# Performance work log

Hardware: AMD Instinct MI355X
Metric: run time of the kernel (lower is better)

Reference implementation:

```python
import jax, jax.numpy as jnp
import numpy as np

N = 8192
E = 131072
IN_DIM = 3000
HID = 512      # gcn1 out = HID // 2 = 256
OUT = 64
EPS = 1e-12


def gcn_conv(x, W, b, src, dst, n):
    """PyG GCNConv: add self-loops, symmetric norm, gather-matmul-scatter."""
    xw = x @ W                                   # [n, out]
    loop = jnp.arange(n, dtype=src.dtype)
    s = jnp.concatenate([src, loop])             # source j
    d = jnp.concatenate([dst, loop])             # target i
    deg = jax.ops.segment_sum(jnp.ones(s.shape[0], dtype=xw.dtype), d, num_segments=n)
    dinv = deg ** -0.5                           # deg >= 1 due to self-loops
    norm = dinv[s] * dinv[d]                     # [E+n]
    out = jax.ops.segment_sum(norm[:, None] * xw[s], d, num_segments=n)
    return out + b


def avg_readout(emb, mask):
    vsum = mask @ emb                            # [N, h]
    row_sum = jnp.sum(mask, axis=1, keepdims=True)
    g = vsum / row_sum
    nrm = jnp.maximum(jnp.linalg.norm(g, axis=1, keepdims=True), EPS)
    return g / nrm                               # F.normalize(p=2, dim=1)


def bilinear(h, c, Wd, bd):
    # nn.Bilinear(n_h, n_h, 1): out[n,o] = sum_ij h[n,i] Wd[o,i,j] c[n,j] + bd[o]
    return jnp.einsum('ni,oij,nj->no', h, Wd, c) + bd


def setup_inputs() -> dict:
    key = jax.random.key(0)
    k1, k2, k3, k4, k5, k6, k7 = jax.random.split(key, 7)
    gene_data = jax.random.normal(k1, (N, IN_DIM), dtype=jnp.float32)
    # sparse binary neighborhood mask (~16 neighbors/row) + self so row sums > 0
    mask = (jax.random.uniform(k2, (N, N)) < (16.0 / N)).astype(jnp.float32)
    mask = jnp.maximum(mask, jnp.eye(N, dtype=jnp.float32))
    spatial_edge_index = jax.random.randint(k3, (2, E), 0, N, dtype=jnp.int64)
    perm = jax.random.permutation(k4, N).astype(jnp.int64)
    h1 = HID // 2
    W1 = jax.random.normal(k5, (IN_DIM, h1), dtype=jnp.float32) / np.sqrt(IN_DIM)
    b1 = jnp.zeros((h1,), dtype=jnp.float32)
    W2 = jax.random.normal(k6, (h1, OUT), dtype=jnp.float32) / np.sqrt(h1)
    b2 = jnp.zeros((OUT,), dtype=jnp.float32)
    Wd = jax.random.normal(k7, (1, OUT, OUT), dtype=jnp.float32) / np.sqrt(OUT)
    bd = jnp.zeros((1,), dtype=jnp.float32)
    return {"gene_data": gene_data, "mask": mask, "W1": W1, "b1": b1,
            "W2": W2, "b2": b2, "Wd": Wd, "bd": bd,
            "spatial_edge_index": spatial_edge_index, "perm": perm}


def reference(gene_data, mask, W1, b1, W2, b2, Wd, bd, spatial_edge_index, perm):
    src, dst = spatial_edge_index[0], spatial_edge_index[1]
    n = gene_data.shape[0]
    x1 = gene_data
    x1_c = gene_data[perm]                       # permuted (corrupted) graph
    # dropout inactive (eval mode, p=0.0)
    x1 = jax.nn.relu(gcn_conv(x1, W1, b1, src, dst, n))
    x1_c = jax.nn.relu(gcn_conv(x1_c, W1, b1, src, dst, n))
    x1 = jax.nn.relu(gcn_conv(x1, W2, b2, src, dst, n))
    x1_c = jax.nn.relu(gcn_conv(x1_c, W2, b2, src, dst, n))
    g1 = jax.nn.sigmoid(avg_readout(x1, mask))
    g1_c = jax.nn.sigmoid(avg_readout(x1_c, mask))
    ret1 = jnp.concatenate([bilinear(x1, g1, Wd, bd), bilinear(x1_c, g1, Wd, bd)], axis=1)
    ret1_c = jnp.concatenate([bilinear(x1_c, g1_c, Wd, bd), bilinear(x1, g1_c, Wd, bd)], axis=1)
    return (x1, ret1, ret1_c)
```

## Files before the change

### kernel.cpp

```cpp
#include <hip/hip_runtime.h>
#include <hip/hip_bf16.h>

#define NN 8192
#define NMASK 8191
#define IND 3000
#define INDP 3008
#define H1 256
#define OUTD 64

typedef __bf16 bf16x8 __attribute__((ext_vector_type(8)));
typedef float floatx4 __attribute__((ext_vector_type(4)));

__device__ __forceinline__ unsigned short f2b(float f) {
    __hip_bfloat16 h = __float2bfloat16(f);
    unsigned short u;
    __builtin_memcpy(&u, &h, 2);
    return u;
}


__global__ void k_probe(float code, float* out) {
    if (threadIdx.x == 0 && blockIdx.x == 0) out[0] = code;
}


__global__ void k_pre(const unsigned* __restrict__ eraw, const unsigned* __restrict__ praw,
                      int* __restrict__ flags, int* __restrict__ deg,
                      const float* __restrict__ W1, const float* __restrict__ W2,
                      __hip_bfloat16* __restrict__ W1t, __hip_bfloat16* __restrict__ W2t) {
    int b = blockIdx.x;
    int t = threadIdx.x;
    if (b < 2) {
        const unsigned* r = (b == 0) ? eraw : praw;
        __shared__ int cnt;
        if (t == 0) cnt = 0;
        __syncthreads();
        int z = 0;
        for (int k = t; k < 2048; k += 256)
            if (r[2 * k + 1] == 0u) z++;
        atomicAdd(&cnt, z);
        __syncthreads();
        if (t == 0) flags[b] = (cnt > 1024) ? 1 : 0;
    } else if (b < 10) {
#pragma unroll
        for (int u = 0; u < 4; ++u) deg[(b - 2) * 1024 + u * 256 + t] = 0;
    } else if (b < 12) {
        int idx = (b - 10) * 256 + t;
#pragma unroll
        for (int u = 0; u < 4; ++u) {
            int k = idx * 4 + u;
            int c = k >> 3;
            int r = 3000 + (k & 7);
            W1t[(size_t)c * INDP + r] = __float2bfloat16(0.f);
        }
    } else {
        int idx = (b - 12) * 256 + t;
        if (idx < IND * H1) {
            int r = idx / H1, c = idx % H1;
            W1t[(size_t)c * INDP + r] = __float2bfloat16(W1[idx]);
        } else {
            int j = idx - IND * H1;
            if (j < H1 * OUTD) {
                int r = j / OUTD, c = j % OUTD;
                W2t[(size_t)c * H1 + r] = __float2bfloat16(W2[j]);
            }
        }
    }
}


__global__ void k_prep(const unsigned* __restrict__ eraw, const unsigned* __restrict__ praw,
                       const int* __restrict__ flags, int* __restrict__ eidx32,
                       int* __restrict__ perm32, int* __restrict__ deg, int E, int n) {
    int i = blockIdx.x * blockDim.x + threadIdx.x;
    if (i < 2 * E) {
        unsigned v = flags[0] ? eraw[2 * (size_t)i] : eraw[i];
        int x = (int)(v & (unsigned)NMASK);
        eidx32[i] = x;
        if (i >= E) atomicAdd(&deg[x], 1);
    } else {
        int j = i - 2 * E;
        if (j < n) {
            unsigned v = flags[1] ? praw[2 * (size_t)j] : praw[j];
            perm32[j] = (int)(v & (unsigned)NMASK);
        }
    }
}


__global__ __launch_bounds__(1024) void k_scan(const int* __restrict__ deg,
                                               int* __restrict__ row_ptr,
                                               int* __restrict__ cursor,
                                               float* __restrict__ dinv, int n) {
    __shared__ int sums[1024];
    int t = threadIdx.x;
    int per = n / 1024;
    int base = t * per;
    int s = 0;
    for (int u = 0; u < per; ++u) s += deg[base + u];
    sums[t] = s;
    __syncthreads();
    for (int off = 1; off < 1024; off <<= 1) {
        int v = (t >= off) ? sums[t - off] : 0;
        __syncthreads();
        sums[t] += v;
        __syncthreads();
    }
    int run = (t == 0) ? 0 : sums[t - 1];
    for (int u = 0; u < per; ++u) {
        int i = base + u;
        row_ptr[i] = run;
        cursor[i] = run;
        int d = deg[i];
        dinv[i] = rsqrtf((float)(1 + d));
        run += d;
    }
    if (t == 1023) row_ptr[n] = run;
}

__global__ void k_scatter(const int* __restrict__ src, const int* __restrict__ dst,
                          int* __restrict__ cursor, int* __restrict__ col, int E) {
    int e = blockIdx.x * blockDim.x + threadIdx.x;
    if (e < E) {
        int d = dst[e];
        int p = atomicAdd(&cursor[d], 1);
        if (p >= 0 && p < E) col[p] = src[e];
    }
}


__global__ __launch_bounds__(256) void k_gemm1(const float* __restrict__ A,
                                               const __hip_bfloat16* __restrict__ Bt,
                                               float* __restrict__ C) {
    __shared__ __align__(16) unsigned short As[64 * 72];
    __shared__ __align__(16) unsigned short Bs[64 * 72];
    int t = threadIdx.x;
    int n0 = blockIdx.x * 64;
    int m0 = blockIdx.y * 64;
    int lane = t & 63;
    int w = t >> 6;
    int srow = t >> 2;
    int schunk = (t & 3) * 16;
    const float* Arow = A + (size_t)(m0 + srow) * IND + schunk;
    const unsigned short* Brow = (const unsigned short*)Bt + (size_t)(n0 + srow) * INDP + schunk;

    floatx4 acc0 = {0.f, 0.f, 0.f, 0.f}, acc1 = acc0, acc2 = acc0, acc3 = acc0;
    int msub = w * 16;
    int arow = msub + (lane & 15);
    int koff = (lane >> 4) * 8;
    int nlo = lane & 15;

    float4 pa0, pa1, pa2, pa3;
    uint4 pb0, pb1;
    auto load_tile = [&](int k0) {
        float4 z4 = make_float4(0.f, 0.f, 0.f, 0.f);
        uint4 zu = make_uint4(0u, 0u, 0u, 0u);
        pa0 = z4; pa1 = z4; pa2 = z4; pa3 = z4; pb0 = zu; pb1 = zu;
        int kk = k0 + schunk;
        if (kk < IND) {
            const float* ap = Arow + k0;
            pa0 = *reinterpret_cast<const float4*>(ap);
            pa1 = *reinterpret_cast<const float4*>(ap + 4);
            pb0 = *reinterpret_cast<const uint4*>(Brow + k0);
        }
        if (kk + 8 < IND) {
            const float* ap = Arow + k0 + 8;
            pa2 = *reinterpret_cast<const float4*>(ap);
            pa3 = *reinterpret_cast<const float4*>(ap + 4);
            pb1 = *reinterpret_cast<const uint4*>(Brow + k0 + 8);
        }
    };
    load_tile(0);
    for (int k0 = 0; k0 < IND; k0 += 64) {
        uint4 av0, av1, bv0 = pb0, bv1 = pb1;
        {
            unsigned short t8[8] = {f2b(pa0.x), f2b(pa0.y), f2b(pa0.z), f2b(pa0.w),
                                    f2b(pa1.x), f2b(pa1.y), f2b(pa1.z), f2b(pa1.w)};
            __builtin_memcpy(&av0, t8, 16);
        }
        {
            unsigned short t8[8] = {f2b(pa2.x), f2b(pa2.y), f2b(pa2.z), f2b(pa2.w),
                                    f2b(pa3.x), f2b(pa3.y), f2b(pa3.z), f2b(pa3.w)};
            __builtin_memcpy(&av1, t8, 16);
        }
        __syncthreads();
        *reinterpret_cast<uint4*>(&As[srow * 72 + schunk]) = av0;
        *reinterpret_cast<uint4*>(&As[srow * 72 + schunk + 8]) = av1;
        *reinterpret_cast<uint4*>(&Bs[srow * 72 + schunk]) = bv0;
        *reinterpret_cast<uint4*>(&Bs[srow * 72 + schunk + 8]) = bv1;
        __syncthreads();
        if (k0 + 64 < IND) load_tile(k0 + 64);
#pragma unroll
        for (int ks = 0; ks < 64; ks += 32) {
            bf16x8 af = *reinterpret_cast<const bf16x8*>(&As[arow * 72 + ks + koff]);
            bf16x8 b0 = *reinterpret_cast<const bf16x8*>(&Bs[(0 + nlo) * 72 + ks + koff]);
            bf16x8 b1 = *reinterpret_cast<const bf16x8*>(&Bs[(16 + nlo) * 72 + ks + koff]);
            bf16x8 b2 = *reinterpret_cast<const bf16x8*>(&Bs[(32 + nlo) * 72 + ks + koff]);
            bf16x8 b3 = *reinterpret_cast<const bf16x8*>(&Bs[(48 + nlo) * 72 + ks + koff]);
            acc0 = __builtin_amdgcn_mfma_f32_16x16x32_bf16(af, b0, acc0, 0, 0, 0);
            acc1 = __builtin_amdgcn_mfma_f32_16x16x32_bf16(af, b1, acc1, 0, 0, 0);
            acc2 = __builtin_amdgcn_mfma_f32_16x16x32_bf16(af, b2, acc2, 0, 0, 0);
            acc3 = __builtin_amdgcn_mfma_f32_16x16x32_bf16(af, b3, acc3, 0, 0, 0);
        }
    }
    int crow = msub + (lane >> 4) * 4;
    int ccol = lane & 15;
    floatx4 accs[4] = {acc0, acc1, acc2, acc3};
#pragma unroll
    for (int j = 0; j < 4; ++j) {
#pragma unroll
        for (int r = 0; r < 4; ++r) {
            C[(size_t)(m0 + crow + r) * H1 + (n0 + j * 16 + ccol)] = accs[j][r];
        }
    }
}


__global__ __launch_bounds__(256) void k_gemm2(const __hip_bfloat16* __restrict__ A,
                                               const __hip_bfloat16* __restrict__ Bt,
                                               float* __restrict__ C,
                                               int M, int N, int K) {
    __shared__ __align__(16) unsigned short As[64 * 40];
    __shared__ __align__(16) unsigned short Bs[64 * 40];
    int t = threadIdx.x;
    int m0 = blockIdx.x * 64;
    int n0 = blockIdx.y * 64;
    int lane = t & 63;
    int w = t >> 6;
    int srow = t >> 2;
    int schunk = (t & 3) * 8;
    size_t aoff = (size_t)(m0 + srow) * K + schunk;
    const unsigned short* Brow = (const unsigned short*)Bt + (size_t)(n0 + srow) * K + schunk;

    floatx4 acc0 = {0.f, 0.f, 0.f, 0.f}, acc1 = acc0, acc2 = acc0, acc3 = acc0;
    int msub = w * 16;
    int arow = msub + (lane & 15);
    int koff = (lane >> 4) * 8;
    int nlo = lane & 15;

    uint4 pa = *reinterpret_cast<const uint4*>((const unsigned short*)A + aoff);
    uint4 pb = *reinterpret_cast<const uint4*>(Brow);
    for (int k0 = 0; k0 < K; k0 += 32) {
        uint4 av = pa, bv = pb;
        __syncthreads();
        *reinterpret_cast<uint4*>(&As[srow * 40 + schunk]) = av;
        *reinterpret_cast<uint4*>(&Bs[srow * 40 + schunk]) = bv;
        __syncthreads();
        if (k0 + 32 < K) {
            pa = *reinterpret_cast<const uint4*>((const unsigned short*)A + aoff + k0 + 32);
            pb = *reinterpret_cast<const uint4*>(Brow + k0 + 32);
        }
        bf16x8 af = *reinterpret_cast<const bf16x8*>(&As[arow * 40 + koff]);
        bf16x8 bf0 = *reinterpret_cast<const bf16x8*>(&Bs[(0 + nlo) * 40 + koff]);
        bf16x8 bf1 = *reinterpret_cast<const bf16x8*>(&Bs[(16 + nlo) * 40 + koff]);
        bf16x8 bf2 = *reinterpret_cast<const bf16x8*>(&Bs[(32 + nlo) * 40 + koff]);
        bf16x8 bf3 = *reinterpret_cast<const bf16x8*>(&Bs[(48 + nlo) * 40 + koff]);
        acc0 = __builtin_amdgcn_mfma_f32_16x16x32_bf16(af, bf0, acc0, 0, 0, 0);
        acc1 = __builtin_amdgcn_mfma_f32_16x16x32_bf16(af, bf1, acc1, 0, 0, 0);
        acc2 = __builtin_amdgcn_mfma_f32_16x16x32_bf16(af, bf2, acc2, 0, 0, 0);
        acc3 = __builtin_amdgcn_mfma_f32_16x16x32_bf16(af, bf3, acc3, 0, 0, 0);
    }
    int crow = msub + (lane >> 4) * 4;
    int ccol = lane & 15;
    floatx4 accs[4] = {acc0, acc1, acc2, acc3};
#pragma unroll
    for (int j = 0; j < 4; ++j) {
#pragma unroll
        for (int r = 0; r < 4; ++r) {
            C[(size_t)(m0 + crow + r) * N + (n0 + j * 16 + ccol)] = accs[j][r];
        }
    }
}


__global__ __launch_bounds__(256) void k_agg1(const float* __restrict__ xw1,
                                              const int* __restrict__ row_ptr,
                                              const int* __restrict__ col,
                                              const float* __restrict__ dinv,
                                              const int* __restrict__ perm,
                                              const float* __restrict__ b1,
                                              __hip_bfloat16* __restrict__ h_all, int n) {
    int lane = threadIdx.x & 63;
    int i = blockIdx.x * 4 + (threadIdx.x >> 6);
    float di = dinv[i];
    int pi = perm[i];
    float sw = di * di;
    int c4 = lane * 4;
    floatx4 acc = sw * *reinterpret_cast<const floatx4*>(xw1 + (size_t)i * H1 + c4);
    floatx4 accc = sw * *reinterpret_cast<const floatx4*>(xw1 + (size_t)pi * H1 + c4);
    int s = row_ptr[i], e = row_ptr[i + 1];
#pragma unroll 4
    for (int t = s; t < e; ++t) {
        int j = col[t];
        float wv = di * dinv[j];
        int pj = perm[j];
        acc += wv * *reinterpret_cast<const floatx4*>(xw1 + (size_t)j * H1 + c4);
        accc += wv * *reinterpret_cast<const floatx4*>(xw1 + (size_t)pj * H1 + c4);
    }
    floatx4 b4 = *reinterpret_cast<const floatx4*>(b1 + c4);
    ushort4 h0, h1;
    h0.x = f2b(fmaxf(acc[0] + b4[0], 0.f));
    h0.y = f2b(fmaxf(acc[1] + b4[1], 0.f));
    h0.z = f2b(fmaxf(acc[2] + b4[2], 0.f));
    h0.w = f2b(fmaxf(acc[3] + b4[3], 0.f));
    h1.x = f2b(fmaxf(accc[0] + b4[0], 0.f));
    h1.y = f2b(fmaxf(accc[1] + b4[1], 0.f));
    h1.z = f2b(fmaxf(accc[2] + b4[2], 0.f));
    h1.w = f2b(fmaxf(accc[3] + b4[3], 0.f));
    *reinterpret_cast<ushort4*>(h_all + (size_t)i * H1 + c4) = h0;
    *reinterpret_cast<ushort4*>(h_all + (size_t)(n + i) * H1 + c4) = h1;
}


__global__ __launch_bounds__(256) void k_agg2(const float* __restrict__ hw_all,
                                              const int* __restrict__ row_ptr,
                                              const int* __restrict__ col,
                                              const float* __restrict__ dinv,
                                              const float* __restrict__ b2,
                                              float* __restrict__ x1_all,
                                              float* __restrict__ out_x1, int n) {
    int lane = threadIdx.x & 63;
    int i = blockIdx.x * 4 + (threadIdx.x >> 6);
    float di = dinv[i];
    float sw = di * di;
    float acc = sw * hw_all[(size_t)i * OUTD + lane];
    float accc = sw * hw_all[(size_t)(n + i) * OUTD + lane];
    int s = row_ptr[i], e = row_ptr[i + 1];
#pragma unroll 4
    for (int t = s; t < e; ++t) {
        int j = col[t];
        float wv = di * dinv[j];
        acc += wv * hw_all[(size_t)j * OUTD + lane];
        accc += wv * hw_all[(size_t)(n + j) * OUTD + lane];
    }
    float b = b2[lane];
    float v = fmaxf(acc + b, 0.f);
    float vc = fmaxf(accc + b, 0.f);
    x1_all[(size_t)i * OUTD + lane] = v;
    x1_all[(size_t)(n + i) * OUTD + lane] = vc;
    out_x1[(size_t)i * OUTD + lane] = v;
}


__global__ __launch_bounds__(256) void k_readout(const float* __restrict__ mask,
                                                 const float* __restrict__ x1_all,
                                                 const float* __restrict__ Wd,
                                                 const float* __restrict__ bd,
                                                 float* __restrict__ ret1,
                                                 float* __restrict__ ret1c, int n) {
    int i = blockIdx.x;
    int lane = threadIdx.x & 63;
    int w = threadIdx.x >> 6;
    float acc = 0.f, accc = 0.f, rs = 0.f;
    const float* mrow = mask + (size_t)i * n;
    int quarter = n >> 2;
    int qbase = w * quarter;
    for (int it = 0; it < 4; ++it) {
        int jb = qbase + it * 512 + lane * 8;
        floatx4 q0 = __builtin_nontemporal_load(reinterpret_cast<const floatx4*>(mrow + jb));
        floatx4 q1 = __builtin_nontemporal_load(reinterpret_cast<const floatx4*>(mrow + jb + 4));
        float qa[8] = {q0[0], q0[1], q0[2], q0[3], q1[0], q1[1], q1[2], q1[3]};
        bool nz = false;
#pragma unroll
        for (int u = 0; u < 8; ++u) nz |= (qa[u] != 0.f);
        unsigned long long bal = __ballot(nz);
        while (bal) {
            int l = __builtin_ctzll(bal);
            bal &= bal - 1;
            int j0 = qbase + it * 512 + l * 8;
#pragma unroll
            for (int u = 0; u < 8; ++u) {
                float m = __shfl(qa[u], l);
                if (m != 0.f) {
                    int j = j0 + u;
                    acc += m * x1_all[(size_t)j * OUTD + lane];
                    accc += m * x1_all[(size_t)(n + j) * OUTD + lane];
                    rs += m;
                }
            }
        }
    }
    __shared__ float sa[4][64], sc[4][64], sr[4];
    sa[w][lane] = acc;
    sc[w][lane] = accc;
    if (lane == 0) sr[w] = rs;
    __syncthreads();
    if (w == 0) {
        float tot = sa[0][lane] + sa[1][lane] + sa[2][lane] + sa[3][lane];
        float totc = sc[0][lane] + sc[1][lane] + sc[2][lane] + sc[3][lane];
        float rst = fmaxf(sr[0] + sr[1] + sr[2] + sr[3], 1e-20f);
        float g = tot / rst;
        float gc = totc / rst;
        float s1 = g * g, s2 = gc * gc;
#pragma unroll
        for (int off = 32; off; off >>= 1) {
            s1 += __shfl_xor(s1, off);
            s2 += __shfl_xor(s2, off);
        }
        float gn = g / fmaxf(sqrtf(s1), 1e-12f);
        float gnc = gc / fmaxf(sqrtf(s2), 1e-12f);
        float gsig = 1.f / (1.f + __expf(-gn));
        float gcsig = 1.f / (1.f + __expf(-gnc));
        float tg = 0.f, tgc = 0.f;
        const float* wrow = Wd + lane * 64;
#pragma unroll 8
        for (int j = 0; j < 64; ++j) {
            float gj = __shfl(gsig, j);
            float gcj = __shfl(gcsig, j);
            float wv = wrow[j];
            tg += wv * gj;
            tgc += wv * gcj;
        }
        float x = x1_all[(size_t)i * OUTD + lane];
        float xc = x1_all[(size_t)(n + i) * OUTD + lane];
        float r0 = x * tg, r1 = xc * tg, r2 = xc * tgc, r3 = x * tgc;
#pragma unroll
        for (int off = 32; off; off >>= 1) {
            r0 += __shfl_down(r0, off);
            r1 += __shfl_down(r1, off);
            r2 += __shfl_down(r2, off);
            r3 += __shfl_down(r3, off);
        }
        if (lane == 0) {
            float b = bd[0];
            ret1[(size_t)i * 2 + 0] = r0 + b;
            ret1[(size_t)i * 2 + 1] = r1 + b;
            ret1c[(size_t)i * 2 + 0] = r2 + b;
            ret1c[(size_t)i * 2 + 1] = r3 + b;
        }
    }
}


extern "C" void kernel_launch(void* const* d_in, const int* in_sizes, int n_in,
                              void* d_out, int out_size, void* d_ws, size_t ws_size,
                              hipStream_t stream) {
    const float* gene = (const float*)d_in[0];
    const float* mask = (const float*)d_in[1];
    const float* W1 = (const float*)d_in[2];
    const float* b1 = (const float*)d_in[3];
    const float* W2 = (const float*)d_in[4];
    const float* b2 = (const float*)d_in[5];
    const float* Wd = (const float*)d_in[6];
    const float* bd = (const float*)d_in[7];
    const unsigned* eidx_raw = (const unsigned*)d_in[8];
    const unsigned* perm_raw = (const unsigned*)d_in[9];
    const int n = NN;
    const int E = in_sizes[8] / 2;

    char* base = (char*)d_ws;
    char* p = base;
    auto alloc = [&](size_t bytes) -> char* {
        char* r = p;
        p += (bytes + 255) & ~(size_t)255;
        return r;
    };
    int* flags = (int*)alloc(256);
    int* eidx32 = (int*)alloc((size_t)2 * E * 4);
    int* perm32 = (int*)alloc((size_t)n * 4);
    int* deg = (int*)alloc((size_t)n * 4);
    int* row_ptr = (int*)alloc((size_t)(n + 1) * 4);
    int* cursor = (int*)alloc((size_t)n * 4);
    float* dinv = (float*)alloc((size_t)n * 4);
    int* col = (int*)alloc((size_t)E * 4);
    __hip_bfloat16* W2t = (__hip_bfloat16*)alloc((size_t)H1 * OUTD * 2);
    __hip_bfloat16* W1t = (__hip_bfloat16*)alloc((size_t)INDP * H1 * 2);
    float* xw1 = (float*)alloc((size_t)n * H1 * 4);
    __hip_bfloat16* h_all = (__hip_bfloat16*)alloc((size_t)2 * n * H1 * 2);
    size_t need = (size_t)(p - base);
    float* hw_all = xw1;
    float* x1_all = xw1 + (size_t)2 * n * OUTD;

    float* out_x1 = (float*)d_out;
    float* out_ret1 = out_x1 + (size_t)n * OUTD;
    float* out_ret1c = out_ret1 + (size_t)n * 2;

    if (ws_size < need) {
        k_probe<<<1, 64, 0, stream>>>(1000.f + (float)(ws_size >> 20), out_x1);
        return;
    }

    k_pre<<<3076, 256, 0, stream>>>(eidx_raw, perm_raw, flags, deg, W1, W2, W1t, W2t);

    k_prep<<<(2 * E + n + 255) / 256, 256, 0, stream>>>(eidx_raw, perm_raw, flags,
                                                        eidx32, perm32, deg, E, n);
    const int* srcv = eidx32;
    const int* dstv = eidx32 + E;

    k_scan<<<1, 1024, 0, stream>>>(deg, row_ptr, cursor, dinv, n);
    k_scatter<<<(E + 255) / 256, 256, 0, stream>>>(srcv, dstv, cursor, col, E);

    k_gemm1<<<dim3(H1 / 64, n / 64), 256, 0, stream>>>(gene, W1t, xw1);

    k_agg1<<<n / 4, 256, 0, stream>>>(xw1, row_ptr, col, dinv, perm32, b1, h_all, n);

    k_gemm2<<<dim3(2 * n / 64, OUTD / 64), 256, 0, stream>>>(h_all, W2t, hw_all, 2 * n, OUTD, H1);

    k_agg2<<<n / 4, 256, 0, stream>>>(hw_all, row_ptr, col, dinv, b2, x1_all, out_x1, n);

    k_readout<<<n, 256, 0, stream>>>(mask, x1_all, Wd, bd, out_ret1, out_ret1c, n);
}
```

Baseline: 609.2 us.

## Pipeline mask rows through an LDS ring and compact nonzeros per wave

```diff
diff --git a/kernel.cpp b/kernel.cpp
--- a/kernel.cpp
+++ b/kernel.cpp
@@ -10,6 +10,9 @@
 
 typedef __bf16 bf16x8 __attribute__((ext_vector_type(8)));
 typedef float floatx4 __attribute__((ext_vector_type(4)));
+
+typedef const __attribute__((address_space(1))) void GV;
+typedef __attribute__((address_space(3))) void LV;
 
 __device__ __forceinline__ unsigned short f2b(float f) {
     __hip_bfloat16 h = __float2bfloat16(f);
@@ -348,86 +351,116 @@
                                                  const float* __restrict__ bd,
                                                  float* __restrict__ ret1,
                                                  float* __restrict__ ret1c, int n) {
-    int i = blockIdx.x;
+    __shared__ __align__(16) float ring[4][4][512];
+    __shared__ uint2 ents[4][256];
     int lane = threadIdx.x & 63;
     int w = threadIdx.x >> 6;
-    float acc = 0.f, accc = 0.f, rs = 0.f;
-    const float* mrow = mask + (size_t)i * n;
-    int quarter = n >> 2;
-    int qbase = w * quarter;
-    for (int it = 0; it < 4; ++it) {
-        int jb = qbase + it * 512 + lane * 8;
-        floatx4 q0 = __builtin_nontemporal_load(reinterpret_cast<const floatx4*>(mrow + jb));
-        floatx4 q1 = __builtin_nontemporal_load(reinterpret_cast<const floatx4*>(mrow + jb + 4));
-        float qa[8] = {q0[0], q0[1], q0[2], q0[3], q1[0], q1[1], q1[2], q1[3]};
-        bool nz = false;
-#pragma unroll
-        for (int u = 0; u < 8; ++u) nz |= (qa[u] != 0.f);
-        unsigned long long bal = __ballot(nz);
-        while (bal) {
-            int l = __builtin_ctzll(bal);
-            bal &= bal - 1;
-            int j0 = qbase + it * 512 + l * 8;
-#pragma unroll
-            for (int u = 0; u < 8; ++u) {
-                float m = __shfl(qa[u], l);
-                if (m != 0.f) {
-                    int j = j0 + u;
-                    acc += m * x1_all[(size_t)j * OUTD + lane];
-                    accc += m * x1_all[(size_t)(n + j) * OUTD + lane];
-                    rs += m;
-                }
+    int row = blockIdx.x * 4 + w;
+    const float* mrow = mask + (size_t)row * n;
+
+    auto issue = [&](int c) {
+        int slot = c & 3;
+        const float* g0 = mrow + c * 512 + lane * 4;
+        __builtin_amdgcn_global_load_lds((GV*)g0, (LV*)&ring[w][slot][0], 16, 0, 0);
+        __builtin_amdgcn_global_load_lds((GV*)(g0 + 256), (LV*)&ring[w][slot][256], 16, 0, 0);
+    };
+    issue(0);
+    issue(1);
+    issue(2);
+
+    int base = 0;
+    float rs = 0.f;
+    unsigned long long below = (lane == 63) ? ~0ull >> 1 : (1ull << lane) - 1;
+    for (int k = 0; k < 16; ++k) {
+        if (k < 13) {
+            issue(k + 3);
+            asm volatile("s_waitcnt vmcnt(6)" ::: "memory");
+        } else if (k == 13) {
+            asm volatile("s_waitcnt vmcnt(4)" ::: "memory");
+        } else if (k == 14) {
+            asm volatile("s_waitcnt vmcnt(2)" ::: "memory");
+        } else {
+            asm volatile("s_waitcnt vmcnt(0)" ::: "memory");
+        }
+        int slot = k & 3;
+        floatx4 q0 = *reinterpret_cast<floatx4*>(&ring[w][slot][lane * 4]);
+        floatx4 q1 = *reinterpret_cast<floatx4*>(&ring[w][slot][256 + lane * 4]);
+        int cb = k * 512 + lane * 4;
+#pragma unroll
+        for (int u = 0; u < 4; ++u) {
+            float v = q0[u];
+            unsigned long long bal = __ballot(v != 0.f);
+            if (v != 0.f) {
+                int r = base + __popcll(bal & below);
+                if (r < 256) ents[w][r] = make_uint2((unsigned)(cb + u), __float_as_uint(v));
+                rs += v;
             }
-        }
-    }
-    __shared__ float sa[4][64], sc[4][64], sr[4];
-    sa[w][lane] = acc;
-    sc[w][lane] = accc;
-    if (lane == 0) sr[w] = rs;
-    __syncthreads();
-    if (w == 0) {
-        float tot = sa[0][lane] + sa[1][lane] + sa[2][lane] + sa[3][lane];
-        float totc = sc[0][lane] + sc[1][lane] + sc[2][lane] + sc[3][lane];
-        float rst = fmaxf(sr[0] + sr[1] + sr[2] + sr[3], 1e-20f);
-        float g = tot / rst;
-        float gc = totc / rst;
-        float s1 = g * g, s2 = gc * gc;
-#pragma unroll
-        for (int off = 32; off; off >>= 1) {
-            s1 += __shfl_xor(s1, off);
-            s2 += __shfl_xor(s2, off);
-        }
-        float gn = g / fmaxf(sqrtf(s1), 1e-12f);
-        float gnc = gc / fmaxf(sqrtf(s2), 1e-12f);
-        float gsig = 1.f / (1.f + __expf(-gn));
-        float gcsig = 1.f / (1.f + __expf(-gnc));
-        float tg = 0.f, tgc = 0.f;
-        const float* wrow = Wd + lane * 64;
+            base += __popcll(bal);
+        }
+#pragma unroll
+        for (int u = 0; u < 4; ++u) {
+            float v = q1[u];
+            unsigned long long bal = __ballot(v != 0.f);
+            if (v != 0.f) {
+                int r = base + __popcll(bal & below);
+                if (r < 256) ents[w][r] = make_uint2((unsigned)(cb + 256 + u), __float_as_uint(v));
+                rs += v;
+            }
+            base += __popcll(bal);
+        }
+    }
+#pragma unroll
+    for (int off = 32; off; off >>= 1) rs += __shfl_xor(rs, off);
+
+    int cnt = min(base, 256);
+    float acc = 0.f, accc = 0.f;
+#pragma unroll 2
+    for (int e = 0; e < cnt; ++e) {
+        uint2 ent = ents[w][e];
+        float m = __uint_as_float(ent.y);
+        int j = (int)ent.x;
+        acc += m * x1_all[(size_t)j * OUTD + lane];
+        accc += m * x1_all[(size_t)(n + j) * OUTD + lane];
+    }
+    float rst = fmaxf(rs, 1e-20f);
+    float g = acc / rst;
+    float gc = accc / rst;
+    float s1 = g * g, s2 = gc * gc;
+#pragma unroll
+    for (int off = 32; off; off >>= 1) {
+        s1 += __shfl_xor(s1, off);
+        s2 += __shfl_xor(s2, off);
+    }
+    float gn = g / fmaxf(sqrtf(s1), 1e-12f);
+    float gnc = gc / fmaxf(sqrtf(s2), 1e-12f);
+    float gsig = 1.f / (1.f + __expf(-gn));
+    float gcsig = 1.f / (1.f + __expf(-gnc));
+    float tg = 0.f, tgc = 0.f;
+    const float* wrow = Wd + lane * 64;
 #pragma unroll 8
-        for (int j = 0; j < 64; ++j) {
-            float gj = __shfl(gsig, j);
-            float gcj = __shfl(gcsig, j);
-            float wv = wrow[j];
-            tg += wv * gj;
-            tgc += wv * gcj;
-        }
-        float x = x1_all[(size_t)i * OUTD + lane];
-        float xc = x1_all[(size_t)(n + i) * OUTD + lane];
-        float r0 = x * tg, r1 = xc * tg, r2 = xc * tgc, r3 = x * tgc;
-#pragma unroll
-        for (int off = 32; off; off >>= 1) {
-            r0 += __shfl_down(r0, off);
-            r1 += __shfl_down(r1, off);
-            r2 += __shfl_down(r2, off);
-            r3 += __shfl_down(r3, off);
-        }
-        if (lane == 0) {
-            float b = bd[0];
-            ret1[(size_t)i * 2 + 0] = r0 + b;
-            ret1[(size_t)i * 2 + 1] = r1 + b;
-            ret1c[(size_t)i * 2 + 0] = r2 + b;
-            ret1c[(size_t)i * 2 + 1] = r3 + b;
-        }
+    for (int j = 0; j < 64; ++j) {
+        float gj = __shfl(gsig, j);
+        float gcj = __shfl(gcsig, j);
+        float wv = wrow[j];
+        tg += wv * gj;
+        tgc += wv * gcj;
+    }
+    float x = x1_all[(size_t)row * OUTD + lane];
+    float xc = x1_all[(size_t)(n + row) * OUTD + lane];
+    float r0 = x * tg, r1 = xc * tg, r2 = xc * tgc, r3 = x * tgc;
+#pragma unroll
+    for (int off = 32; off; off >>= 1) {
+        r0 += __shfl_down(r0, off);
+        r1 += __shfl_down(r1, off);
+        r2 += __shfl_down(r2, off);
+        r3 += __shfl_down(r3, off);
+    }
+    if (lane == 0) {
+        float b = bd[0];
+        ret1[(size_t)row * 2 + 0] = r0 + b;
+        ret1[(size_t)row * 2 + 1] = r1 + b;
+        ret1c[(size_t)row * 2 + 0] = r2 + b;
+        ret1c[(size_t)row * 2 + 1] = r3 + b;
     }
 }
 
@@ -498,5 +531,5 @@
 
     k_agg2<<<n / 4, 256, 0, stream>>>(hw_all, row_ptr, col, dinv, b2, x1_all, out_x1, n);
 
-    k_readout<<<n, 256, 0, stream>>>(mask, x1_all, Wd, bd, out_ret1, out_ret1c, n);
-}
+    k_readout<<<n / 4, 256, 0, stream>>>(mask, x1_all, Wd, bd, out_ret1, out_ret1c, n);
+}
```

Result: no change. 610.0 us (+0.1%).
